# Optimization experiments

Hardware: AMD Instinct MI355X
Metric: run time of the kernel (lower is better)

Reference implementation:

```python
import jax, jax.numpy as jnp
import numpy as np

NEG_INF = -9e15  # same masking constant as the torch module


def setup_inputs() -> dict:
    key = jax.random.key(0)
    k1, k2, k3 = jax.random.split(key, 3)
    B, S, F = 8, 2048, 128
    H, D = 4, 32  # n_heads, head_dim = out_features // n_heads
    features = jax.random.normal(k1, (B, S, F), dtype=jnp.float32)
    adj_matrix = jax.random.randint(k2, (B, S, S), 0, 2, dtype=jnp.int32)
    # Xavier-uniform-ish init for W [H, F, D]
    limit = float(np.sqrt(6.0 / (F + D)))
    W = jax.random.uniform(k3, (H, F, D), dtype=jnp.float32, minval=-limit, maxval=limit)
    return {"features": features, "adj_matrix": adj_matrix, "W": W}


def reference(features, adj_matrix, W):
    # features: [B, S, F], adj_matrix: [B, S, S] (>0 == edge), W: [H, F, D]
    D = W.shape[-1]
    Wh = jnp.einsum("bsf,hfd->bhsd", features, W)                 # [B, H, S, D]
    scores = jnp.einsum("bhsd,bhtd->bhst", Wh, Wh) / jnp.sqrt(jnp.float32(D))
    scores = jnp.where(adj_matrix[:, None, :, :] > 0, scores, NEG_INF)
    attn = jax.nn.softmax(scores, axis=-1)                         # [B, H, S, S]
    # dropout is identity at inference (training=False)
    h = jnp.einsum("bhst,bhtd->bhsd", attn, Wh)                    # [B, H, S, D]
    B, H, S, _ = h.shape
    # concat heads along feature dim, matching torch.cat(heads, dim=2)
    return jnp.transpose(h, (0, 2, 1, 3)).reshape(B, S, H * D)
```

## Files before the change

kernel.cpp:

```cpp
#include <hip/hip_runtime.h>
#include <hip/hip_bf16.h>
#include <stdint.h>


namespace {
constexpr int S = 2048;
constexpr int F = 128;
constexpr int H = 4;
constexpr int D = 32;

typedef __attribute__((ext_vector_type(4))) float f32x4;
typedef __attribute__((ext_vector_type(8))) short s16x8;
typedef __attribute__((ext_vector_type(4))) short s16x4;

__device__ __forceinline__ short f2bf(float f) {
  __hip_bfloat16 h = __float2bfloat16(f);
  short s; __builtin_memcpy(&s, &h, sizeof(s)); return s;
}
__device__ __forceinline__ float bf2f(short s) {
  __hip_bfloat16 h; __builtin_memcpy(&h, &s, sizeof(s));
  return __bfloat162float(h);
}
__device__ __forceinline__ unsigned pkbf(float a, float b) {
  __hip_bfloat162 h = __float22bfloat162_rn(float2{a, b});
  unsigned u; __builtin_memcpy(&u, &h, 4); return u;
}

__global__ __launch_bounds__(256) void gat_proj(const float* __restrict__ feat,
                                                const float* __restrict__ W,
                                                short* __restrict__ Wh,
                                                short* __restrict__ WhT) {
  __shared__ __align__(16) short ftile[64][136];
  const int tid = threadIdx.x;
  const int w = tid >> 6;
  const int l = tid & 63;
  const int ln = l & 15, lg = l >> 4, g4 = (l >> 4) * 4;
  const int row0 = blockIdx.x * 64;
  const int b = row0 >> 11;
  const int sl0 = row0 & (S - 1);

#pragma unroll
  for (int i = 0; i < 4; ++i) {
    int c = i * 256 + tid;
    int r = c >> 4, c8 = (c & 15) * 8;
    const float* src = feat + (size_t)(row0 + r) * F + c8;
    float4 v0 = *(const float4*)src;
    float4 v1 = *(const float4*)(src + 4);
    s16x8 v;
    v[0]=f2bf(v0.x); v[1]=f2bf(v0.y); v[2]=f2bf(v0.z); v[3]=f2bf(v0.w);
    v[4]=f2bf(v1.x); v[5]=f2bf(v1.y); v[6]=f2bf(v1.z); v[7]=f2bf(v1.w);
    *(s16x8*)&ftile[r][c8] = v;
  }

  s16x8 bfr[4][2];
#pragma unroll
  for (int ks = 0; ks < 4; ++ks)
#pragma unroll
    for (int nt = 0; nt < 2; ++nt) {
      s16x8 v;
#pragma unroll
      for (int j = 0; j < 8; ++j)
        v[j] = f2bf(W[((size_t)w * F + ks*32 + lg*8 + j) * D + nt*16 + ln]);
      bfr[ks][nt] = v;
    }
  __syncthreads();

  const f32x4 z4 = {0.f, 0.f, 0.f, 0.f};
#pragma unroll
  for (int mt = 0; mt < 4; ++mt) {
    s16x8 a[4];
#pragma unroll
    for (int ks = 0; ks < 4; ++ks)
      a[ks] = *(const s16x8*)&ftile[mt*16 + ln][ks*32 + lg*8];
#pragma unroll
    for (int nt = 0; nt < 2; ++nt) {
      f32x4 c = z4;
#pragma unroll
      for (int ks = 0; ks < 4; ++ks)
        c = __builtin_amdgcn_mfma_f32_16x16x32_bf16(a[ks], bfr[ks][nt], c, 0, 0, 0);
      s16x4 tv;
#pragma unroll
      for (int r = 0; r < 4; ++r) {
        tv[r] = f2bf(c[r]);
        int srow = row0 + mt*16 + g4 + r;
        int s = srow & (S - 1);
        Wh[(((size_t)b * H + w) * S + s) * D + nt*16 + ln] = tv[r];
      }
      *(s16x4*)&WhT[(((size_t)b * H + w) * D + nt*16 + ln) * S + sl0 + mt*16 + g4] = tv;
    }
  }
}

__global__ __launch_bounds__(256, 3) void gat_attn(const int* __restrict__ adj,
                                                   const short* __restrict__ Wh,
                                                   const short* __restrict__ WhT,
                                                   float* __restrict__ out,
                                                   float* __restrict__ PO,
                                                   float* __restrict__ PS,
                                                   int tiles) {
  __shared__ __align__(16) unsigned short maskm[2][32][72];
  __shared__ __align__(16) short ptl[H][32][64];

  const int tid = threadIdx.x;
  const int w = tid >> 6;
  const int l = tid & 63;
  const int ln = l & 15, lg = l >> 4, g4 = (l >> 4) * 4;
  const int e3 = ln & 7;
  const int lh = lg & 1;

  const int N = gridDim.x;
  const int rbid = ((int)blockIdx.x & 7) * (N >> 3) + ((int)blockIdx.x >> 3);
  const int c = rbid >> 9;
  const int g = rbid & 511;
  const int b = g >> 6;
  const int s0 = (g & 63) * 32;
  const int it0 = c * tiles;

  const short* WhBH = Wh + ((size_t)b * H + w) * S * D;
  const short* WhTBH = WhT + ((size_t)b * H + w) * D * S;
  short* pw = &ptl[w][0][0];

  const int arow = tid >> 3;
  const int gc = tid & 7;
  const int* adjR = adj + (size_t)b * S * S + (size_t)(s0 + arow) * S
                    + (size_t)it0 * 64 + gc * 8;

  const float cs = 0.25503486f;
  s16x8 qf[2];
#pragma unroll
  for (int qt = 0; qt < 2; ++qt) {
    s16x8 v = *(const s16x8*)&WhBH[(size_t)(s0 + qt*16 + ln) * D + lg*8];
    s16x8 o;
#pragma unroll
    for (int j = 0; j < 8; ++j) o[j] = f2bf(bf2f(v[j]) * cs);
    qf[qt] = o;
  }

  s16x8 onesf;
#pragma unroll
  for (int j = 0; j < 8; ++j) onesf[j] = (short)0x3F80;

  const f32x4 z4 = {0.f, 0.f, 0.f, 0.f};
  f32x4 accO[2][2];
  f32x4 accP[2];
#pragma unroll
  for (int i = 0; i < 2; ++i) {
    accP[i] = z4;
#pragma unroll
    for (int j = 0; j < 2; ++j) accO[i][j] = z4;
  }

  {
    int4 a0 = *(const int4*)adjR;
    int4 a1 = *(const int4*)(adjR + 4);
    uint4 mw;
    mw.x = (a0.x ? 0xFFFFu : 0u) | (a0.y ? 0xFFFF0000u : 0u);
    mw.y = (a0.z ? 0xFFFFu : 0u) | (a0.w ? 0xFFFF0000u : 0u);
    mw.z = (a1.x ? 0xFFFFu : 0u) | (a1.y ? 0xFFFF0000u : 0u);
    mw.w = (a1.z ? 0xFFFFu : 0u) | (a1.w ? 0xFFFF0000u : 0u);
    *(uint4*)&maskm[0][arow][gc * 8] = mw;
  }
  s16x8 kf[4];
  s16x8 av[2][2];
  {
    const size_t t0 = (size_t)it0 * 64;
#pragma unroll
    for (int mt = 0; mt < 4; ++mt)
      kf[mt] = *(const s16x8*)&WhBH[(t0 + mt*16 + ln) * D + lg*8];
#pragma unroll
    for (int dt = 0; dt < 2; ++dt)
#pragma unroll
      for (int kt = 0; kt < 2; ++kt)
        av[dt][kt] = *(const s16x8*)&WhTBH[(size_t)(dt*16 + ln) * S + t0 + kt*32 + lg*8];
  }
  __syncthreads();

#pragma unroll 1
  for (int i = 0; i < tiles; ++i) {
    const int cur = i & 1;
    const bool pf = (i + 1 < tiles);
    const int iLd = pf ? i + 1 : i;
    const size_t tnl = (size_t)(it0 + iLd) * 64;

    int4 a0n = *(const int4*)(adjR + (size_t)iLd * 64);
    int4 a1n = *(const int4*)(adjR + (size_t)iLd * 64 + 4);

#pragma unroll
    for (int mt = 0; mt < 4; ++mt) {
      f32x4 sA = __builtin_amdgcn_mfma_f32_16x16x32_bf16(kf[mt], qf[0], z4, 0, 0, 0);
      f32x4 sB = __builtin_amdgcn_mfma_f32_16x16x32_bf16(kf[mt], qf[1], z4, 0, 0, 0);
      kf[mt] = *(const s16x8*)&WhBH[(tnl + mt*16 + ln) * D + lg*8];

      const int pgo = ((mt*2 + (lg >> 1)) ^ e3) * 8 + lh * 4;
      {
        uint2 mm = *(const uint2*)&maskm[cur][ln][mt*16 + g4];
        float p0 = __builtin_amdgcn_exp2f(sA[0]);
        float p1 = __builtin_amdgcn_exp2f(sA[1]);
        float p2 = __builtin_amdgcn_exp2f(sA[2]);
        float p3 = __builtin_amdgcn_exp2f(sA[3]);
        uint2 pk;
        pk.x = pkbf(p0, p1) & mm.x;
        pk.y = pkbf(p2, p3) & mm.y;
        *(uint2*)&pw[ln*64 + pgo] = pk;
      }
      {
        uint2 mm = *(const uint2*)&maskm[cur][16 + ln][mt*16 + g4];
        float p0 = __builtin_amdgcn_exp2f(sB[0]);
        float p1 = __builtin_amdgcn_exp2f(sB[1]);
        float p2 = __builtin_amdgcn_exp2f(sB[2]);
        float p3 = __builtin_amdgcn_exp2f(sB[3]);
        uint2 pk;
        pk.x = pkbf(p0, p1) & mm.x;
        pk.y = pkbf(p2, p3) & mm.y;
        *(uint2*)&pw[(16 + ln)*64 + pgo] = pk;
      }
    }

    s16x8 ap[2][2];
#pragma unroll
    for (int qt = 0; qt < 2; ++qt)
#pragma unroll
      for (int kt = 0; kt < 2; ++kt)
        ap[qt][kt] = *(const s16x8*)&pw[(qt*16 + ln)*64 + (((kt*4 + lg) ^ e3) << 3)];

#pragma unroll
    for (int dt = 0; dt < 2; ++dt)
#pragma unroll
      for (int qt = 0; qt < 2; ++qt)
#pragma unroll
        for (int kt = 0; kt < 2; ++kt)
          accO[dt][qt] = __builtin_amdgcn_mfma_f32_16x16x32_bf16(
              av[dt][kt], ap[qt][kt], accO[dt][qt], 0, 0, 0);

#pragma unroll
    for (int dt = 0; dt < 2; ++dt)
#pragma unroll
      for (int kt = 0; kt < 2; ++kt)
        av[dt][kt] = *(const s16x8*)&WhTBH[(size_t)(dt*16 + ln) * S + tnl + kt*32 + lg*8];

#pragma unroll
    for (int qt = 0; qt < 2; ++qt)
#pragma unroll
      for (int kt = 0; kt < 2; ++kt)
        accP[qt] = __builtin_amdgcn_mfma_f32_16x16x32_bf16(
            onesf, ap[qt][kt], accP[qt], 0, 0, 0);

    if (pf) {
      uint4 mw;
      mw.x = (a0n.x ? 0xFFFFu : 0u) | (a0n.y ? 0xFFFF0000u : 0u);
      mw.y = (a0n.z ? 0xFFFFu : 0u) | (a0n.w ? 0xFFFF0000u : 0u);
      mw.z = (a1n.x ? 0xFFFFu : 0u) | (a1n.y ? 0xFFFF0000u : 0u);
      mw.w = (a1n.z ? 0xFFFFu : 0u) | (a1n.w ? 0xFFFF0000u : 0u);
      *(uint4*)&maskm[cur ^ 1][arow][gc * 8] = mw;
    }
    __syncthreads();
  }

  if (PO == nullptr) {
#pragma unroll
    for (int qt = 0; qt < 2; ++qt) {
      float inv = 1.0f / accP[qt][0];
#pragma unroll
      for (int dt = 0; dt < 2; ++dt) {
        f32x4 o;
#pragma unroll
        for (int r = 0; r < 4; ++r) o[r] = accO[dt][qt][r] * inv;
        *(f32x4*)&out[((size_t)b * S + s0 + qt*16 + ln) * (H * D) + w*32 + dt*16 + g4] = o;
      }
    }
  } else {
    const size_t pbase = (size_t)rbid * H + w;
    float* po = PO + pbase * 1024;
#pragma unroll
    for (int qt = 0; qt < 2; ++qt) {
#pragma unroll
      for (int dt = 0; dt < 2; ++dt)
        *(f32x4*)&po[(qt*16 + ln)*32 + dt*16 + g4] = accO[dt][qt];
      if (lg == 0) PS[pbase * 32 + qt*16 + ln] = accP[qt][0];
    }
  }
}

__global__ __launch_bounds__(256) void gat_reduce(const float* __restrict__ PO,
                                                  const float* __restrict__ PS,
                                                  float* __restrict__ out,
                                                  int nchunks) {
  const int f4 = blockIdx.x * 256 + threadIdx.x;
  const int d4 = f4 & 31;
  const int h = d4 >> 3;
  const int dq = d4 & 7;
  const int s_flat = f4 >> 5;
  const int b = s_flat >> 11, s = s_flat & 2047;
  const int g = b * 64 + (s >> 5), q = s & 31;

  f32x4 acc = {0.f, 0.f, 0.f, 0.f};
  float ps = 0.f;
  for (int c = 0; c < nchunks; ++c) {
    size_t pbase = ((size_t)(c * 512 + g)) * H + h;
    acc += *(const f32x4*)&PO[pbase * 1024 + q*32 + dq*4];
    ps += PS[pbase * 32 + q];
  }
  float inv = 1.0f / ps;
  f32x4 o = acc * inv;
  *(f32x4*)&out[(size_t)f4 * 4] = o;
}

}

extern "C" void kernel_launch(void* const* d_in, const int* in_sizes, int n_in,
                              void* d_out, int out_size, void* d_ws, size_t ws_size,
                              hipStream_t stream) {
  const float* feat = (const float*)d_in[0];
  const int* adj    = (const int*)d_in[1];
  const float* W    = (const float*)d_in[2];
  float* out        = (float*)d_out;

  short* Wh  = (short*)d_ws;
  short* WhT = Wh + (size_t)8 * H * S * D;
  const size_t whbytes = (size_t)2 * 8 * H * S * D * sizeof(short);
  const size_t chunkPO = (size_t)512 * H * 1024 * sizeof(float);
  const size_t chunkPS = (size_t)512 * H * 32 * sizeof(float);

  int nchunks = 1;
  if (ws_size >= whbytes + 2 * (chunkPO + chunkPS)) nchunks = 2;

  float* PO = nullptr;
  float* PS = nullptr;
  if (nchunks > 1) {
    PO = (float*)((char*)d_ws + whbytes);
    PS = (float*)((char*)d_ws + whbytes + (size_t)nchunks * chunkPO);
  }

  gat_proj<<<(8 * S) / 64, 256, 0, stream>>>(feat, W, Wh, WhT);
  gat_attn<<<512 * nchunks, 256, 0, stream>>>(adj, Wh, WhT, out, PO, PS, 32 / nchunks);
  if (nchunks > 1) gat_reduce<<<2048, 256, 0, stream>>>(PO, PS, out, nchunks);
}
```

Measured before the change: 76.02 us.

## Split attention block into 8 waves, one per head and query half

The attention kernel now launches 512 threads per block, with each wave handling one head and one 16-row query half instead of one head and all 32 rows. This halves the per-wave MFMA and register work and is meant to raise occupancy and latency hiding. The row-sum MFMA against a ones vector is dropped; instead the masked bf16 probabilities are summed in VALU and reduced across lanes with shuffles. The cost is that every wave must reload its K and V fragments, doubling the global/L2 traffic for those operands, and more waves take part in each block barrier.

```diff
diff --git a/kernel.cpp b/kernel.cpp
--- a/kernel.cpp
+++ b/kernel.cpp
@@ -91,7 +91,7 @@
   }
 }
 
-__global__ __launch_bounds__(256, 3) void gat_attn(const int* __restrict__ adj,
+__global__ __launch_bounds__(512, 8) void gat_attn(const int* __restrict__ adj,
                                                    const short* __restrict__ Wh,
                                                    const short* __restrict__ WhT,
                                                    float* __restrict__ out,
@@ -99,10 +99,12 @@
                                                    float* __restrict__ PS,
                                                    int tiles) {
   __shared__ __align__(16) unsigned short maskm[2][32][72];
-  __shared__ __align__(16) short ptl[H][32][64];
+  __shared__ __align__(16) short ptl[8][16][64];
 
   const int tid = threadIdx.x;
-  const int w = tid >> 6;
+  const int ww = tid >> 6;
+  const int h = ww >> 1;
+  const int qtw = ww & 1;
   const int l = tid & 63;
   const int ln = l & 15, lg = l >> 4, g4 = (l >> 4) * 4;
   const int e3 = ln & 7;
@@ -116,49 +118,34 @@
   const int s0 = (g & 63) * 32;
   const int it0 = c * tiles;
 
-  const short* WhBH = Wh + ((size_t)b * H + w) * S * D;
-  const short* WhTBH = WhT + ((size_t)b * H + w) * D * S;
-  short* pw = &ptl[w][0][0];
-
-  const int arow = tid >> 3;
-  const int gc = tid & 7;
-  const int* adjR = adj + (size_t)b * S * S + (size_t)(s0 + arow) * S
-                    + (size_t)it0 * 64 + gc * 8;
+  const short* WhBH = Wh + ((size_t)b * H + h) * S * D;
+  const short* WhTBH = WhT + ((size_t)b * H + h) * D * S;
+  short* pw = &ptl[ww][0][0];
+
+  const int arow = tid >> 4;
+  const int c4 = (tid & 15) * 4;
+  const int* adjTh = adj + (size_t)b * S * S + (size_t)(s0 + arow) * S
+                     + (size_t)it0 * 64 + c4;
 
   const float cs = 0.25503486f;
-  s16x8 qf[2];
-#pragma unroll
-  for (int qt = 0; qt < 2; ++qt) {
-    s16x8 v = *(const s16x8*)&WhBH[(size_t)(s0 + qt*16 + ln) * D + lg*8];
-    s16x8 o;
-#pragma unroll
-    for (int j = 0; j < 8; ++j) o[j] = f2bf(bf2f(v[j]) * cs);
-    qf[qt] = o;
-  }
-
-  s16x8 onesf;
-#pragma unroll
-  for (int j = 0; j < 8; ++j) onesf[j] = (short)0x3F80;
+  s16x8 qf;
+  {
+    s16x8 v = *(const s16x8*)&WhBH[(size_t)(s0 + qtw*16 + ln) * D + lg*8];
+#pragma unroll
+    for (int j = 0; j < 8; ++j) qf[j] = f2bf(bf2f(v[j]) * cs);
+  }
 
   const f32x4 z4 = {0.f, 0.f, 0.f, 0.f};
-  f32x4 accO[2][2];
-  f32x4 accP[2];
-#pragma unroll
-  for (int i = 0; i < 2; ++i) {
-    accP[i] = z4;
-#pragma unroll
-    for (int j = 0; j < 2; ++j) accO[i][j] = z4;
-  }
+  f32x4 accO[2];
+  accO[0] = z4; accO[1] = z4;
+  float psum = 0.f;
 
   {
-    int4 a0 = *(const int4*)adjR;
-    int4 a1 = *(const int4*)(adjR + 4);
-    uint4 mw;
-    mw.x = (a0.x ? 0xFFFFu : 0u) | (a0.y ? 0xFFFF0000u : 0u);
-    mw.y = (a0.z ? 0xFFFFu : 0u) | (a0.w ? 0xFFFF0000u : 0u);
-    mw.z = (a1.x ? 0xFFFFu : 0u) | (a1.y ? 0xFFFF0000u : 0u);
-    mw.w = (a1.z ? 0xFFFFu : 0u) | (a1.w ? 0xFFFF0000u : 0u);
-    *(uint4*)&maskm[0][arow][gc * 8] = mw;
+    int4 a = *(const int4*)adjTh;
+    uint2 mw;
+    mw.x = (a.x ? 0xFFFFu : 0u) | (a.y ? 0xFFFF0000u : 0u);
+    mw.y = (a.z ? 0xFFFFu : 0u) | (a.w ? 0xFFFF0000u : 0u);
+    *(uint2*)&maskm[0][arow][c4] = mw;
   }
   s16x8 kf[4];
   s16x8 av[2][2];
@@ -182,55 +169,41 @@
     const int iLd = pf ? i + 1 : i;
     const size_t tnl = (size_t)(it0 + iLd) * 64;
 
-    int4 a0n = *(const int4*)(adjR + (size_t)iLd * 64);
-    int4 a1n = *(const int4*)(adjR + (size_t)iLd * 64 + 4);
+    int4 an = *(const int4*)(adjTh + (size_t)iLd * 64);
 
 #pragma unroll
     for (int mt = 0; mt < 4; ++mt) {
-      f32x4 sA = __builtin_amdgcn_mfma_f32_16x16x32_bf16(kf[mt], qf[0], z4, 0, 0, 0);
-      f32x4 sB = __builtin_amdgcn_mfma_f32_16x16x32_bf16(kf[mt], qf[1], z4, 0, 0, 0);
+      f32x4 sv = __builtin_amdgcn_mfma_f32_16x16x32_bf16(kf[mt], qf, z4, 0, 0, 0);
       kf[mt] = *(const s16x8*)&WhBH[(tnl + mt*16 + ln) * D + lg*8];
 
+      uint2 mm = *(const uint2*)&maskm[cur][qtw*16 + ln][mt*16 + g4];
+      float p0 = __builtin_amdgcn_exp2f(sv[0]);
+      float p1 = __builtin_amdgcn_exp2f(sv[1]);
+      float p2 = __builtin_amdgcn_exp2f(sv[2]);
+      float p3 = __builtin_amdgcn_exp2f(sv[3]);
+      uint2 pk;
+      pk.x = pkbf(p0, p1) & mm.x;
+      pk.y = pkbf(p2, p3) & mm.y;
+      float m0 = bf2f((short)(pk.x & 0xFFFFu));
+      float m1 = bf2f((short)(pk.x >> 16));
+      float m2 = bf2f((short)(pk.y & 0xFFFFu));
+      float m3 = bf2f((short)(pk.y >> 16));
+      psum += (m0 + m1) + (m2 + m3);
       const int pgo = ((mt*2 + (lg >> 1)) ^ e3) * 8 + lh * 4;
-      {
-        uint2 mm = *(const uint2*)&maskm[cur][ln][mt*16 + g4];
-        float p0 = __builtin_amdgcn_exp2f(sA[0]);
-        float p1 = __builtin_amdgcn_exp2f(sA[1]);
-        float p2 = __builtin_amdgcn_exp2f(sA[2]);
-        float p3 = __builtin_amdgcn_exp2f(sA[3]);
-        uint2 pk;
-        pk.x = pkbf(p0, p1) & mm.x;
-        pk.y = pkbf(p2, p3) & mm.y;
-        *(uint2*)&pw[ln*64 + pgo] = pk;
-      }
-      {
-        uint2 mm = *(const uint2*)&maskm[cur][16 + ln][mt*16 + g4];
-        float p0 = __builtin_amdgcn_exp2f(sB[0]);
-        float p1 = __builtin_amdgcn_exp2f(sB[1]);
-        float p2 = __builtin_amdgcn_exp2f(sB[2]);
-        float p3 = __builtin_amdgcn_exp2f(sB[3]);
-        uint2 pk;
-        pk.x = pkbf(p0, p1) & mm.x;
-        pk.y = pkbf(p2, p3) & mm.y;
-        *(uint2*)&pw[(16 + ln)*64 + pgo] = pk;
-      }
-    }
-
-    s16x8 ap[2][2];
-#pragma unroll
-    for (int qt = 0; qt < 2; ++qt)
+      *(uint2*)&pw[ln*64 + pgo] = pk;
+    }
+
+    s16x8 ap[2];
+#pragma unroll
+    for (int kt = 0; kt < 2; ++kt)
+      ap[kt] = *(const s16x8*)&pw[ln*64 + (((kt*4 + lg) ^ e3) << 3)];
+
+#pragma unroll
+    for (int dt = 0; dt < 2; ++dt)
 #pragma unroll
       for (int kt = 0; kt < 2; ++kt)
-        ap[qt][kt] = *(const s16x8*)&pw[(qt*16 + ln)*64 + (((kt*4 + lg) ^ e3) << 3)];
-
-#pragma unroll
-    for (int dt = 0; dt < 2; ++dt)
-#pragma unroll
-      for (int qt = 0; qt < 2; ++qt)
-#pragma unroll
-        for (int kt = 0; kt < 2; ++kt)
-          accO[dt][qt] = __builtin_amdgcn_mfma_f32_16x16x32_bf16(
-              av[dt][kt], ap[qt][kt], accO[dt][qt], 0, 0, 0);
+        accO[dt] = __builtin_amdgcn_mfma_f32_16x16x32_bf16(
+            av[dt][kt], ap[kt], accO[dt], 0, 0, 0);
 
 #pragma unroll
     for (int dt = 0; dt < 2; ++dt)
@@ -238,46 +211,34 @@
       for (int kt = 0; kt < 2; ++kt)
         av[dt][kt] = *(const s16x8*)&WhTBH[(size_t)(dt*16 + ln) * S + tnl + kt*32 + lg*8];
 
-#pragma unroll
-    for (int qt = 0; qt < 2; ++qt)
-#pragma unroll
-      for (int kt = 0; kt < 2; ++kt)
-        accP[qt] = __builtin_amdgcn_mfma_f32_16x16x32_bf16(
-            onesf, ap[qt][kt], accP[qt], 0, 0, 0);
-
     if (pf) {
-      uint4 mw;
-      mw.x = (a0n.x ? 0xFFFFu : 0u) | (a0n.y ? 0xFFFF0000u : 0u);
-      mw.y = (a0n.z ? 0xFFFFu : 0u) | (a0n.w ? 0xFFFF0000u : 0u);
-      mw.z = (a1n.x ? 0xFFFFu : 0u) | (a1n.y ? 0xFFFF0000u : 0u);
-      mw.w = (a1n.z ? 0xFFFFu : 0u) | (a1n.w ? 0xFFFF0000u : 0u);
-      *(uint4*)&maskm[cur ^ 1][arow][gc * 8] = mw;
+      uint2 mw;
+      mw.x = (an.x ? 0xFFFFu : 0u) | (an.y ? 0xFFFF0000u : 0u);
+      mw.y = (an.z ? 0xFFFFu : 0u) | (an.w ? 0xFFFF0000u : 0u);
+      *(uint2*)&maskm[cur ^ 1][arow][c4] = mw;
     }
     __syncthreads();
   }
 
+  psum += __shfl_xor(psum, 16, 64);
+  psum += __shfl_xor(psum, 32, 64);
+
   if (PO == nullptr) {
-#pragma unroll
-    for (int qt = 0; qt < 2; ++qt) {
-      float inv = 1.0f / accP[qt][0];
-#pragma unroll
-      for (int dt = 0; dt < 2; ++dt) {
-        f32x4 o;
-#pragma unroll
-        for (int r = 0; r < 4; ++r) o[r] = accO[dt][qt][r] * inv;
-        *(f32x4*)&out[((size_t)b * S + s0 + qt*16 + ln) * (H * D) + w*32 + dt*16 + g4] = o;
-      }
+    float inv = 1.0f / psum;
+#pragma unroll
+    for (int dt = 0; dt < 2; ++dt) {
+      f32x4 o;
+#pragma unroll
+      for (int r = 0; r < 4; ++r) o[r] = accO[dt][r] * inv;
+      *(f32x4*)&out[((size_t)b * S + s0 + qtw*16 + ln) * (H * D) + h*32 + dt*16 + g4] = o;
     }
   } else {
-    const size_t pbase = (size_t)rbid * H + w;
+    const size_t pbase = (size_t)rbid * H + h;
     float* po = PO + pbase * 1024;
 #pragma unroll
-    for (int qt = 0; qt < 2; ++qt) {
-#pragma unroll
-      for (int dt = 0; dt < 2; ++dt)
-        *(f32x4*)&po[(qt*16 + ln)*32 + dt*16 + g4] = accO[dt][qt];
-      if (lg == 0) PS[pbase * 32 + qt*16 + ln] = accP[qt][0];
-    }
+    for (int dt = 0; dt < 2; ++dt)
+      *(f32x4*)&po[(qtw*16 + ln)*32 + dt*16 + g4] = accO[dt];
+    if (lg == 0) PS[pbase * 32 + qtw*16 + ln] = psum;
   }
 }
 
@@ -332,6 +293,6 @@
   }
 
   gat_proj<<<(8 * S) / 64, 256, 0, stream>>>(feat, W, Wh, WhT);
-  gat_attn<<<512 * nchunks, 256, 0, stream>>>(adj, Wh, WhT, out, PO, PS, 32 / nchunks);
+  gat_attn<<<512 * nchunks, 512, 0, stream>>>(adj, Wh, WhT, out, PO, PS, 32 / nchunks);
   if (nchunks > 1) gat_reduce<<<2048, 256, 0, stream>>>(PO, PS, out, nchunks);
 }
```

Result: slower. 201.1 us (+164.5%).

## Keep softmax probabilities in registers by permuting key rows to match MFMA fragments

Applied to the files above, without the earlier changes.

Reorders which key rows each lane loads into the score MFMA, so the probability outputs already sit in the operand layout of the P·V MFMA. This removes the per-wave LDS staging buffer for P, along with its stores, reads and swizzle. The mask tile is re-padded and written in two 8-byte halves to match the new access pattern. With less LDS and fewer registers, launch bounds go from 3 to 4 blocks per SM, which risks register spills.

```diff
diff --git a/kernel.cpp b/kernel.cpp
--- a/kernel.cpp
+++ b/kernel.cpp
@@ -24,6 +24,11 @@
 __device__ __forceinline__ unsigned pkbf(float a, float b) {
   __hip_bfloat162 h = __float22bfloat162_rn(float2{a, b});
   unsigned u; __builtin_memcpy(&u, &h, 4); return u;
+}
+__device__ __forceinline__ s16x8 mkfrag(uint2 a, uint2 b) {
+  union { unsigned u[4]; s16x8 s; } x;
+  x.u[0] = a.x; x.u[1] = a.y; x.u[2] = b.x; x.u[3] = b.y;
+  return x.s;
 }
 
 __global__ __launch_bounds__(256) void gat_proj(const float* __restrict__ feat,
@@ -91,22 +96,19 @@
   }
 }
 
-__global__ __launch_bounds__(256, 3) void gat_attn(const int* __restrict__ adj,
+__global__ __launch_bounds__(256, 4) void gat_attn(const int* __restrict__ adj,
                                                    const short* __restrict__ Wh,
                                                    const short* __restrict__ WhT,
                                                    float* __restrict__ out,
                                                    float* __restrict__ PO,
                                                    float* __restrict__ PS,
                                                    int tiles) {
-  __shared__ __align__(16) unsigned short maskm[2][32][72];
-  __shared__ __align__(16) short ptl[H][32][64];
+  __shared__ __align__(16) unsigned short maskm[2][32][76];
 
   const int tid = threadIdx.x;
   const int w = tid >> 6;
   const int l = tid & 63;
   const int ln = l & 15, lg = l >> 4, g4 = (l >> 4) * 4;
-  const int e3 = ln & 7;
-  const int lh = lg & 1;
 
   const int N = gridDim.x;
   const int rbid = ((int)blockIdx.x & 7) * (N >> 3) + ((int)blockIdx.x >> 3);
@@ -118,12 +120,16 @@
 
   const short* WhBH = Wh + ((size_t)b * H + w) * S * D;
   const short* WhTBH = WhT + ((size_t)b * H + w) * D * S;
-  short* pw = &ptl[w][0][0];
 
   const int arow = tid >> 3;
   const int gc = tid & 7;
-  const int* adjR = adj + (size_t)b * S * S + (size_t)(s0 + arow) * S
-                    + (size_t)it0 * 64 + gc * 8;
+  const int* adjTh = adj + (size_t)b * S * S + (size_t)(s0 + arow) * S
+                     + (size_t)it0 * 64 + gc * 8;
+
+  int toff[4];
+#pragma unroll
+  for (int mt = 0; mt < 4; ++mt)
+    toff[mt] = 32*(mt >> 1) + 8*(ln >> 2) + 4*(mt & 1) + (ln & 3);
 
   const float cs = 0.25503486f;
   s16x8 qf[2];
@@ -151,14 +157,15 @@
   }
 
   {
-    int4 a0 = *(const int4*)adjR;
-    int4 a1 = *(const int4*)(adjR + 4);
-    uint4 mw;
-    mw.x = (a0.x ? 0xFFFFu : 0u) | (a0.y ? 0xFFFF0000u : 0u);
-    mw.y = (a0.z ? 0xFFFFu : 0u) | (a0.w ? 0xFFFF0000u : 0u);
-    mw.z = (a1.x ? 0xFFFFu : 0u) | (a1.y ? 0xFFFF0000u : 0u);
-    mw.w = (a1.z ? 0xFFFFu : 0u) | (a1.w ? 0xFFFF0000u : 0u);
-    *(uint4*)&maskm[0][arow][gc * 8] = mw;
+    int4 a0 = *(const int4*)adjTh;
+    int4 a1 = *(const int4*)(adjTh + 4);
+    uint2 u0, u1;
+    u0.x = (a0.x ? 0xFFFFu : 0u) | (a0.y ? 0xFFFF0000u : 0u);
+    u0.y = (a0.z ? 0xFFFFu : 0u) | (a0.w ? 0xFFFF0000u : 0u);
+    u1.x = (a1.x ? 0xFFFFu : 0u) | (a1.y ? 0xFFFF0000u : 0u);
+    u1.y = (a1.z ? 0xFFFFu : 0u) | (a1.w ? 0xFFFF0000u : 0u);
+    *(uint2*)&maskm[0][arow][gc * 8] = u0;
+    *(uint2*)&maskm[0][arow][gc * 8 + 4] = u1;
   }
   s16x8 kf[4];
   s16x8 av[2][2];
@@ -166,7 +173,7 @@
     const size_t t0 = (size_t)it0 * 64;
 #pragma unroll
     for (int mt = 0; mt < 4; ++mt)
-      kf[mt] = *(const s16x8*)&WhBH[(t0 + mt*16 + ln) * D + lg*8];
+      kf[mt] = *(const s16x8*)&WhBH[(t0 + toff[mt]) * D + lg*8];
 #pragma unroll
     for (int dt = 0; dt < 2; ++dt)
 #pragma unroll
@@ -182,38 +189,26 @@
     const int iLd = pf ? i + 1 : i;
     const size_t tnl = (size_t)(it0 + iLd) * 64;
 
-    int4 a0n = *(const int4*)(adjR + (size_t)iLd * 64);
-    int4 a1n = *(const int4*)(adjR + (size_t)iLd * 64 + 4);
-
+    int4 a0n = *(const int4*)(adjTh + (size_t)iLd * 64);
+    int4 a1n = *(const int4*)(adjTh + (size_t)iLd * 64 + 4);
+
+    uint2 pks[2][4];
 #pragma unroll
     for (int mt = 0; mt < 4; ++mt) {
       f32x4 sA = __builtin_amdgcn_mfma_f32_16x16x32_bf16(kf[mt], qf[0], z4, 0, 0, 0);
       f32x4 sB = __builtin_amdgcn_mfma_f32_16x16x32_bf16(kf[mt], qf[1], z4, 0, 0, 0);
-      kf[mt] = *(const s16x8*)&WhBH[(tnl + mt*16 + ln) * D + lg*8];
-
-      const int pgo = ((mt*2 + (lg >> 1)) ^ e3) * 8 + lh * 4;
-      {
-        uint2 mm = *(const uint2*)&maskm[cur][ln][mt*16 + g4];
-        float p0 = __builtin_amdgcn_exp2f(sA[0]);
-        float p1 = __builtin_amdgcn_exp2f(sA[1]);
-        float p2 = __builtin_amdgcn_exp2f(sA[2]);
-        float p3 = __builtin_amdgcn_exp2f(sA[3]);
-        uint2 pk;
-        pk.x = pkbf(p0, p1) & mm.x;
-        pk.y = pkbf(p2, p3) & mm.y;
-        *(uint2*)&pw[ln*64 + pgo] = pk;
-      }
-      {
-        uint2 mm = *(const uint2*)&maskm[cur][16 + ln][mt*16 + g4];
-        float p0 = __builtin_amdgcn_exp2f(sB[0]);
-        float p1 = __builtin_amdgcn_exp2f(sB[1]);
-        float p2 = __builtin_amdgcn_exp2f(sB[2]);
-        float p3 = __builtin_amdgcn_exp2f(sB[3]);
-        uint2 pk;
-        pk.x = pkbf(p0, p1) & mm.x;
-        pk.y = pkbf(p2, p3) & mm.y;
-        *(uint2*)&pw[(16 + ln)*64 + pgo] = pk;
-      }
+      kf[mt] = *(const s16x8*)&WhBH[(tnl + toff[mt]) * D + lg*8];
+
+      const int tb = 32*(mt >> 1) + 8*lg + 4*(mt & 1);
+      uint2 mmA = *(const uint2*)&maskm[cur][ln][tb];
+      uint2 mmB = *(const uint2*)&maskm[cur][16 + ln][tb];
+      uint2 pa, pb;
+      pa.x = pkbf(__builtin_amdgcn_exp2f(sA[0]), __builtin_amdgcn_exp2f(sA[1])) & mmA.x;
+      pa.y = pkbf(__builtin_amdgcn_exp2f(sA[2]), __builtin_amdgcn_exp2f(sA[3])) & mmA.y;
+      pb.x = pkbf(__builtin_amdgcn_exp2f(sB[0]), __builtin_amdgcn_exp2f(sB[1])) & mmB.x;
+      pb.y = pkbf(__builtin_amdgcn_exp2f(sB[2]), __builtin_amdgcn_exp2f(sB[3])) & mmB.y;
+      pks[0][mt] = pa;
+      pks[1][mt] = pb;
     }
 
     s16x8 ap[2][2];
@@ -221,7 +216,7 @@
     for (int qt = 0; qt < 2; ++qt)
 #pragma unroll
       for (int kt = 0; kt < 2; ++kt)
-        ap[qt][kt] = *(const s16x8*)&pw[(qt*16 + ln)*64 + (((kt*4 + lg) ^ e3) << 3)];
+        ap[qt][kt] = mkfrag(pks[qt][2*kt], pks[qt][2*kt + 1]);
 
 #pragma unroll
     for (int dt = 0; dt < 2; ++dt)
@@ -246,12 +241,13 @@
             onesf, ap[qt][kt], accP[qt], 0, 0, 0);
 
     if (pf) {
-      uint4 mw;
-      mw.x = (a0n.x ? 0xFFFFu : 0u) | (a0n.y ? 0xFFFF0000u : 0u);
-      mw.y = (a0n.z ? 0xFFFFu : 0u) | (a0n.w ? 0xFFFF0000u : 0u);
-      mw.z = (a1n.x ? 0xFFFFu : 0u) | (a1n.y ? 0xFFFF0000u : 0u);
-      mw.w = (a1n.z ? 0xFFFFu : 0u) | (a1n.w ? 0xFFFF0000u : 0u);
-      *(uint4*)&maskm[cur ^ 1][arow][gc * 8] = mw;
+      uint2 u0, u1;
+      u0.x = (a0n.x ? 0xFFFFu : 0u) | (a0n.y ? 0xFFFF0000u : 0u);
+      u0.y = (a0n.z ? 0xFFFFu : 0u) | (a0n.w ? 0xFFFF0000u : 0u);
+      u1.x = (a1n.x ? 0xFFFFu : 0u) | (a1n.y ? 0xFFFF0000u : 0u);
+      u1.y = (a1n.z ? 0xFFFFu : 0u) | (a1n.w ? 0xFFFF0000u : 0u);
+      *(uint2*)&maskm[cur ^ 1][arow][gc * 8] = u0;
+      *(uint2*)&maskm[cur ^ 1][arow][gc * 8 + 4] = u1;
     }
     __syncthreads();
   }
```

New measurement: 73.32 us. -3.6%, faster.
